# Kernel tuning notes

Measured on AMD Instinct MI355X. Metric: run time of the kernel, lower is better.

## Reference

```python
import jax, jax.numpy as jnp
import numpy as np

B, T, TR, DIM, H = 1, 4096, 1024, 1536, 12
DH = DIM // H          # 128
EPS = 1e-6             # RMSNorm eps
REF_SCALE = 1.0


def setup_inputs() -> dict:
    key = jax.random.key(0)
    ks = jax.random.split(key, 20)
    s = 0.02
    w = lambda k: jax.random.normal(k, (DIM, DIM), jnp.float32) * s
    b = lambda k: jax.random.normal(k, (DIM,), jnp.float32) * 0.01
    theta = jax.random.uniform(ks[2], (T, DH // 2), jnp.float32) * (2.0 * np.pi)
    return {
        "hidden_states": jax.random.normal(ks[0], (B, T, DIM), jnp.float32),
        "ref_hidden_states": jax.random.normal(ks[1], (B, TR, DIM), jnp.float32),
        "rot_cos": jnp.cos(theta),
        "rot_sin": jnp.sin(theta),
        "Wq": w(ks[3]), "bq": b(ks[4]),
        "Wk": w(ks[5]), "bk": b(ks[6]),
        "Wv": w(ks[7]), "bv": b(ks[8]),
        "Wkr": w(ks[9]), "bkr": b(ks[10]),
        "Wvr": w(ks[11]), "bvr": b(ks[12]),
        "Wo": w(ks[13]), "bo": b(ks[14]),
        "gq": jnp.ones((DIM,), jnp.float32),
        "gk": jnp.ones((DIM,), jnp.float32),
    }


def _rmsnorm(x, g):
    return x * jax.lax.rsqrt(jnp.mean(x * x, axis=-1, keepdims=True) + EPS) * g


def _heads(x):  # [B, T, DIM] -> [B, H, T, DH]
    return x.reshape(B, -1, H, DH).transpose(0, 2, 1, 3)


def _merge(x):  # [B, H, T, DH] -> [B, T, DIM]
    return x.transpose(0, 2, 1, 3).reshape(B, -1, DIM)


def _rope(x, c, s):
    # consecutive pairs along DH form complex numbers (view_as_complex semantics)
    xe, xo = x[..., 0::2], x[..., 1::2]
    c = c[None, None]  # [1,1,T,DH/2]
    s = s[None, None]
    re = xe * c - xo * s
    im = xe * s + xo * c
    return jnp.stack([re, im], axis=-1).reshape(x.shape)


def _attn(q, k, v):
    scale = 1.0 / jnp.sqrt(jnp.asarray(DH, q.dtype))
    p = jax.nn.softmax(jnp.einsum("bhqd,bhkd->bhqk", q, k) * scale, axis=-1)
    return jnp.einsum("bhqk,bhkd->bhqd", p, v)


def reference(hidden_states, ref_hidden_states, rot_cos, rot_sin,
              Wq, bq, Wk, bk, Wv, bv, Wkr, bkr, Wvr, bvr, Wo, bo, gq, gk):
    # QKV projections (self-attention: encoder_hidden_states = hidden_states)
    q_lin = hidden_states @ Wq + bq
    k_lin = hidden_states @ Wk + bk
    v_lin = hidden_states @ Wv + bv

    # ---- reference-attention branch (uses pre-RoPE query) ----
    ref_q = _heads(_rmsnorm(q_lin, gq))
    ref_k = _heads(_rmsnorm(ref_hidden_states @ Wkr + bkr, gk))
    ref_v = _heads(ref_hidden_states @ Wvr + bvr)
    ref_out = _merge(_attn(ref_q, ref_k, ref_v))  # [B, T, DIM]

    # ---- main attention with QK-norm + RoPE ----
    q = _rope(_heads(_rmsnorm(q_lin, gq)), rot_cos, rot_sin)
    k = _rope(_heads(_rmsnorm(k_lin, gk)), rot_cos, rot_sin)
    v = _heads(v_lin)
    main_out = _merge(_attn(q, k, v))  # [B, T, DIM]

    # scaled residual combine + output projection (dropout = identity)
    out = main_out + REF_SCALE * ref_out
    return out @ Wo + bo
```

## Files before the change

kernel.cpp:

```cpp
#include <hip/hip_runtime.h>

typedef unsigned short u16;
typedef unsigned int u32;
typedef __attribute__((ext_vector_type(8))) short short8;
typedef __attribute__((ext_vector_type(4))) float f32x4;

__device__ inline u16 f2b(float f) {
  u32 u = __builtin_bit_cast(u32, f);
  u += 0x7fff + ((u >> 16) & 1);
  return (u16)(u >> 16);
}
__device__ inline float b2f(u16 u) {
  return __builtin_bit_cast(float, (u32)u << 16);
}
__device__ inline u32 pack_bf16_rn(float a, float b) {
  const u32 ua = __builtin_bit_cast(u32, a) + 0x8000u;
  const u32 ub = __builtin_bit_cast(u32, b) + 0x8000u;
  return (ua >> 16) | (ub & 0xffff0000u);
}
__device__ inline void c_store(float* p, float v) { *p = v; }
__device__ inline void c_store(u16* p, float v) { *p = f2b(v); }

__device__ inline float fexp2(float x) {
#if __has_builtin(__builtin_amdgcn_exp2f)
  return __builtin_amdgcn_exp2f(x);
#else
  return exp2f(x);
#endif
}

typedef const __attribute__((address_space(1))) u32 gu32;
typedef __attribute__((address_space(3))) u32 lu32;
__device__ inline void async16(const u16* g, u16* l) {
  __builtin_amdgcn_global_load_lds((gu32*)g, (lu32*)l, 16, 0, 0);
}

#define QS (0.08838834764831843f * 1.4426950408889634f)

template <int MI, typename TC>
__global__ __launch_bounds__(256) void gemm128_kernel(
    const u16* __restrict__ A, long lda,
    const u16* __restrict__ Bt, long ldb,
    TC* __restrict__ C0, TC* __restrict__ C1, TC* __restrict__ C2, long ldc,
    const float* b0, const float* b1, const float* b2,
    int K) {
  __shared__ u16 As[32 * MI * 32];
  __shared__ u16 Bs[128 * 32];

  const int tid = threadIdx.x;
  const int lane = tid & 63;
  const int w = tid >> 6;
  const int r = lane & 15;
  const int quad = lane >> 4;
  const int m0 = blockIdx.y * (32 * MI);
  const int nb = blockIdx.x * 128;
  const int seg = nb / 1536;
  const int nc = nb - seg * 1536;
  TC* C = seg == 0 ? C0 : (seg == 1 ? C1 : C2);
  const float* bias = seg == 0 ? b0 : (seg == 1 ? b1 : b2);

  const int srow = lane >> 2;
  const int sx = ((lane & 3) ^ (srow & 3)) * 8;
  const u16* Ag = A + (size_t)(m0 + w * 8 * MI + srow) * lda + sx;
  const u16* Bg = Bt + (size_t)(nb + w * 32 + srow) * ldb + sx;
  u16* Al[MI / 2];
#pragma unroll
  for (int j = 0; j < MI / 2; ++j) Al[j] = &As[(w * 8 * MI + 16 * j) * 32];
  u16* const Bl0 = &Bs[(w * 32) * 32];
  u16* const Bl1 = &Bs[(w * 32 + 16) * 32];

  const int wm = (w >> 1) * (16 * MI);
  const int wn = (w & 1) * 64;

  f32x4 acc[MI][4];
#pragma unroll
  for (int i = 0; i < MI; ++i)
#pragma unroll
    for (int j = 0; j < 4; ++j) acc[i][j] = (f32x4){0.f, 0.f, 0.f, 0.f};

  const int fco = (quad ^ (r & 3)) * 8;

  for (int kk = 0; kk < K; kk += 32) {
    __syncthreads();
#pragma unroll
    for (int j = 0; j < MI / 2; ++j) async16(Ag + kk + (size_t)(16 * j) * lda, Al[j]);
    async16(Bg + kk, Bl0);
    async16(Bg + kk + 16 * ldb, Bl1);
    __syncthreads();

    short8 af[MI], bf[4];
#pragma unroll
    for (int mi = 0; mi < MI; ++mi)
      af[mi] = *reinterpret_cast<const short8*>(&As[(wm + 16 * mi + r) * 32 + fco]);
#pragma unroll
    for (int ni = 0; ni < 4; ++ni)
      bf[ni] = *reinterpret_cast<const short8*>(&Bs[(wn + 16 * ni + r) * 32 + fco]);
#pragma unroll
    for (int mi = 0; mi < MI; ++mi)
#pragma unroll
      for (int ni = 0; ni < 4; ++ni)
        acc[mi][ni] = __builtin_amdgcn_mfma_f32_16x16x32_bf16(af[mi], bf[ni], acc[mi][ni], 0, 0, 0);
  }

#pragma unroll
  for (int mi = 0; mi < MI; ++mi)
#pragma unroll
    for (int ni = 0; ni < 4; ++ni)
#pragma unroll
      for (int rr = 0; rr < 4; ++rr) {
        const int row = m0 + wm + 16 * mi + 4 * quad + rr;
        const int col = nc + wn + 16 * ni + r;
        c_store(&C[(size_t)row * ldc + col], acc[mi][ni][rr] + bias[col]);
      }
}

__global__ __launch_bounds__(256) void conv2_kernel(
    const float* __restrict__ xa, u16* __restrict__ ya, int n8a,
    const float* __restrict__ xb, u16* __restrict__ yb, int n8b) {
  int i = blockIdx.x * 256 + threadIdx.x;
  const float* x;
  u16* y;
  if (i < n8a) {
    x = xa; y = ya;
  } else {
    i -= n8a;
    if (i >= n8b) return;
    x = xb; y = yb;
  }
  const float4 v0 = reinterpret_cast<const float4*>(x)[2 * i];
  const float4 v1 = reinterpret_cast<const float4*>(x)[2 * i + 1];
  uint4 rv;
  rv.x = (u32)f2b(v0.x) | ((u32)f2b(v0.y) << 16);
  rv.y = (u32)f2b(v0.z) | ((u32)f2b(v0.w) << 16);
  rv.z = (u32)f2b(v1.x) | ((u32)f2b(v1.y) << 16);
  rv.w = (u32)f2b(v1.z) | ((u32)f2b(v1.w) << 16);
  reinterpret_cast<uint4*>(y)[i] = rv;
}

__device__ inline void transconv_body(const float* __restrict__ W, u16* __restrict__ Wt) {
  __shared__ u16 Ls[64 * 72];
  const int tid = threadIdx.x;
  const int k0 = blockIdx.y * 64;
  const int n0 = blockIdx.x * 64;
#pragma unroll
  for (int i = 0; i < 4; ++i) {
    const int c = tid + 256 * i;
    const int row = c >> 4;
    const int c4 = (c & 15) * 4;
    const float4 v = *reinterpret_cast<const float4*>(&W[(size_t)(k0 + row) * 1536 + n0 + c4]);
    Ls[(c4 + 0) * 72 + row] = f2b(v.x);
    Ls[(c4 + 1) * 72 + row] = f2b(v.y);
    Ls[(c4 + 2) * 72 + row] = f2b(v.z);
    Ls[(c4 + 3) * 72 + row] = f2b(v.w);
  }
  __syncthreads();
#pragma unroll
  for (int i = 0; i < 2; ++i) {
    const int c = tid + 256 * i;
    const int n = c >> 3;
    const int kc = (c & 7) * 8;
    u16 tmp[8];
#pragma unroll
    for (int j = 0; j < 8; ++j) tmp[j] = Ls[n * 72 + kc + j];
    *reinterpret_cast<uint4*>(&Wt[(size_t)(n0 + n) * 1536 + k0 + kc]) =
        *reinterpret_cast<const uint4*>(tmp);
  }
}

__global__ __launch_bounds__(256) void transconv6_kernel(
    const float* W0, const float* W1, const float* W2,
    const float* W3, const float* W4, const float* W5,
    u16* T0, u16* T1, u16* T2, u16* T3, u16* T4, u16* T5) {
  const int z = blockIdx.z;
  const float* W = z == 0 ? W0 : z == 1 ? W1 : z == 2 ? W2 : z == 3 ? W3 : z == 4 ? W4 : W5;
  u16* Wt = z == 0 ? T0 : z == 1 ? T1 : z == 2 ? T2 : z == 3 ? T3 : z == 4 ? T4 : T5;
  transconv_body(W, Wt);
}

__global__ __launch_bounds__(256) void rmsnorm3_kernel(
    const u16* xq, const u16* xk, const u16* xkr,
    const float* gq, const float* gk,
    const float* rc, const float* rs,
    u16* oq_plain, u16* oq_rope, u16* ok_rope, u16* okr_plain) {
  __shared__ float red[4];
  const int z = blockIdx.y;
  const int row = blockIdx.x;
  if (z == 2 && row >= 1024) return;
  const u16* x; const float* g; u16* po; u16* pr; float sc;
  if (z == 0)      { x = xq;  g = gq; po = oq_plain; pr = oq_rope; sc = QS;  }
  else if (z == 1) { x = xk;  g = gk; po = nullptr;  pr = ok_rope; sc = 1.f; }
  else             { x = xkr; g = gk; po = okr_plain; pr = nullptr; sc = 1.f; }

  const int tid = threadIdx.x;
  const u32* xr = reinterpret_cast<const u32*>(x + (size_t)row * 1536);
  float xe[3], xo[3];
  float ss = 0.f;
#pragma unroll
  for (int j = 0; j < 3; ++j) {
    const u32 u = xr[tid + 256 * j];
    const float e = b2f((u16)(u & 0xffff));
    const float o = b2f((u16)(u >> 16));
    xe[j] = e; xo[j] = o;
    ss += e * e + o * o;
  }
#pragma unroll
  for (int off = 32; off; off >>= 1) ss += __shfl_xor(ss, off, 64);
  if ((tid & 63) == 0) red[tid >> 6] = ss;
  __syncthreads();
  const float total = red[0] + red[1] + red[2] + red[3];
  const float rinv = rsqrtf(total * (1.0f / 1536.0f) + 1e-6f) * sc;
  u32* po32 = po ? reinterpret_cast<u32*>(po + (size_t)row * 1536) : nullptr;
  u32* pr32 = pr ? reinterpret_cast<u32*>(pr + (size_t)row * 1536) : nullptr;
#pragma unroll
  for (int j = 0; j < 3; ++j) {
    const int p = tid + 256 * j;
    const float2 gg = reinterpret_cast<const float2*>(g)[p];
    const float e = xe[j] * rinv * gg.x;
    const float o = xo[j] * rinv * gg.y;
    if (po32) po32[p] = (u32)f2b(e) | ((u32)f2b(o) << 16);
    if (pr32) {
      const int i = p & 63;
      const float c = rc[row * 64 + i];
      const float s = rs[row * 64 + i];
      const float re = e * c - o * s;
      const float im = e * s + o * c;
      pr32[p] = (u32)f2b(re) | ((u32)f2b(im) << 16);
    }
  }
}

__global__ __launch_bounds__(256) void vtrans2_kernel(
    const u16* __restrict__ V0, u16* __restrict__ Vt0,
    const u16* __restrict__ V1, u16* __restrict__ Vt1) {
  __shared__ u16 Ls[64 * 136];
  const int z = blockIdx.z;
  const int kvLen = z == 0 ? 4096 : 1024;
  const int kv0 = blockIdx.x * 64;
  if (kv0 >= kvLen) return;
  const u16* V = z == 0 ? V0 : V1;
  u16* Vt = z == 0 ? Vt0 : Vt1;
  const int tid = threadIdx.x;
  const int h = blockIdx.y;
#pragma unroll
  for (int i = 0; i < 4; ++i) {
    const int c = tid + 256 * i;
    const int row = c >> 4, c8 = c & 15;
    *reinterpret_cast<uint4*>(&Ls[row * 136 + 8 * c8]) =
        *reinterpret_cast<const uint4*>(V + (size_t)(kv0 + row) * 1536 + h * 128 + 8 * c8);
  }
  __syncthreads();
#pragma unroll
  for (int i = 0; i < 4; ++i) {
    const int c = tid + 256 * i;
    const int d = c >> 3, kc = c & 7;
    u16 tmp[8];
#pragma unroll
    for (int j = 0; j < 8; ++j) tmp[j] = Ls[(8 * kc + j) * 136 + d];
    *reinterpret_cast<uint4*>(Vt + ((size_t)h * 128 + d) * kvLen + kv0 + 8 * kc) =
        *reinterpret_cast<const uint4*>(tmp);
  }
}

__global__ __launch_bounds__(256) void flash2_kernel(
    const u16* __restrict__ Qc, const u16* __restrict__ Kc, const u16* __restrict__ Vtc,
    const u16* __restrict__ Qm, const u16* __restrict__ Km, const u16* __restrict__ Vtm,
    u16* __restrict__ Ob) {
  __shared__ u16 Ks[64 * 128];
  __shared__ u16 Vs[128 * 64];
  __shared__ u16 Pb[4][16 * 72];
  __shared__ float ab[4][16];

  const int tid = threadIdx.x;
  const int lane = tid & 63;
  const int w = tid >> 6;
  const int r = lane & 15;
  const int quad = lane >> 4;
  const int h = blockIdx.y;
  const int q0 = blockIdx.x * 64;
  const int qrow = q0 + 16 * w + r;
  const int sw = r & 7;

  f32x4 Ox[8];
#pragma unroll
  for (int dt = 0; dt < 8; ++dt) Ox[dt] = (f32x4){0.f, 0.f, 0.f, 0.f};

  for (int ph = 0; ph < 2; ++ph) {
    const u16* Q  = ph ? Qm : Qc;
    const u16* K  = ph ? Km : Kc;
    const u16* Vt = ph ? Vtm : Vtc;
    const int kvLen = ph ? 4096 : 1024;
    const int nt = kvLen >> 6;

    short8 qf[4];
    {
      const u16* qbase = Q + (size_t)qrow * 1536 + h * 128 + 8 * quad;
#pragma unroll
      for (int ks = 0; ks < 4; ++ks)
        qf[ks] = *reinterpret_cast<const short8*>(qbase + 32 * ks);
    }

    const u16* Vth = Vt + (size_t)h * 128 * kvLen;
    const u16* kg[4]; const u16* vg[4];
    u16* kl[4]; u16* vl[4];
    {
      const int p16 = lane & 15, rin = lane >> 4;
      const int p8 = lane & 7, din = lane >> 3;
#pragma unroll
      for (int j = 0; j < 4; ++j) {
        const int row = 16 * w + 4 * j + rin;
        kg[j] = K + (size_t)row * 1536 + h * 128 + 8 * (p16 ^ (row & 15));
        kl[j] = &Ks[(16 * w + 4 * j) * 128];
        const int d = 32 * w + 8 * j + din;
        vg[j] = Vth + (size_t)d * kvLen + 8 * (p8 ^ (d & 7));
        vl[j] = &Vs[(32 * w + 8 * j) * 64];
      }
    }

    f32x4 Oc[8];
#pragma unroll
    for (int dt = 0; dt < 8; ++dt) Oc[dt] = (f32x4){0.f, 0.f, 0.f, 0.f};
    float m_i = -1e30f, l_i = 0.f;

    for (int t = 0; t < nt; ++t) {
      __syncthreads();
      {
        const size_t ko = (size_t)t * 64 * 1536;
        const int vo = t * 64;
#pragma unroll
        for (int j = 0; j < 4; ++j) async16(kg[j] + ko, kl[j]);
#pragma unroll
        for (int j = 0; j < 4; ++j) async16(vg[j] + vo, vl[j]);
      }
      __syncthreads();

      f32x4 St[4];
#pragma unroll
      for (int mt = 0; mt < 4; ++mt) St[mt] = (f32x4){0.f, 0.f, 0.f, 0.f};
#pragma unroll
      for (int mt = 0; mt < 4; ++mt) {
        const u16* kp = &Ks[(16 * mt + r) * 128];
#pragma unroll
        for (int ks = 0; ks < 4; ++ks) {
          const short8 af = *reinterpret_cast<const short8*>(kp + 8 * ((quad + 4 * ks) ^ r));
          St[mt] = __builtin_amdgcn_mfma_f32_16x16x32_bf16(af, qf[ks], St[mt], 0, 0, 0);
        }
      }

      float mloc = -1e30f;
#pragma unroll
      for (int mt = 0; mt < 4; ++mt)
#pragma unroll
        for (int rr = 0; rr < 4; ++rr) mloc = fmaxf(mloc, St[mt][rr]);
      mloc = fmaxf(mloc, __shfl_xor(mloc, 16, 64));
      mloc = fmaxf(mloc, __shfl_xor(mloc, 32, 64));
      const float mn = fmaxf(m_i, mloc);

      float alpha = 1.0f;
      if (__any(mloc > m_i)) {
        alpha = fexp2(m_i - mn);
        if (quad == 0) ab[w][r] = alpha;
        const float4 a4 = *reinterpret_cast<const float4*>(&ab[w][4 * quad]);
#pragma unroll
        for (int dt = 0; dt < 8; ++dt) {
          Oc[dt][0] *= a4.x; Oc[dt][1] *= a4.y; Oc[dt][2] *= a4.z; Oc[dt][3] *= a4.w;
        }
      }

      float psum = 0.f;
      uint2 pk[4];
#pragma unroll
      for (int mt = 0; mt < 4; ++mt) {
        const float p0 = fexp2(St[mt][0] - mn);
        const float p1 = fexp2(St[mt][1] - mn);
        const float p2 = fexp2(St[mt][2] - mn);
        const float p3 = fexp2(St[mt][3] - mn);
        psum += (p0 + p1) + (p2 + p3);
        pk[mt].x = pack_bf16_rn(p0, p1);
        pk[mt].y = pack_bf16_rn(p2, p3);
      }
      psum += __shfl_xor(psum, 16, 64);
      psum += __shfl_xor(psum, 32, 64);
      l_i = l_i * alpha + psum;
      m_i = mn;

#pragma unroll
      for (int mt = 0; mt < 4; ++mt)
        *reinterpret_cast<uint2*>(&Pb[w][r * 72 + 16 * mt + 4 * quad]) = pk[mt];

      const short8 pa0 = *reinterpret_cast<const short8*>(&Pb[w][r * 72 + 8 * quad]);
      const short8 pa1 = *reinterpret_cast<const short8*>(&Pb[w][r * 72 + 32 + 8 * quad]);

#pragma unroll
      for (int dt = 0; dt < 8; ++dt) {
        const int d = 16 * dt + r;
        const short8 b0 = *reinterpret_cast<const short8*>(&Vs[d * 64 + 8 * (quad ^ sw)]);
        const short8 b1 = *reinterpret_cast<const short8*>(&Vs[d * 64 + 8 * ((4 + quad) ^ sw)]);
        Oc[dt] = __builtin_amdgcn_mfma_f32_16x16x32_bf16(pa0, b0, Oc[dt], 0, 0, 0);
        Oc[dt] = __builtin_amdgcn_mfma_f32_16x16x32_bf16(pa1, b1, Oc[dt], 0, 0, 0);
      }
    }

    if (quad == 0) ab[w][r] = 1.0f / l_i;
    const float4 li4 = *reinterpret_cast<const float4*>(&ab[w][4 * quad]);
    const float lv[4] = {li4.x, li4.y, li4.z, li4.w};
    if (ph == 0) {
#pragma unroll
      for (int dt = 0; dt < 8; ++dt)
#pragma unroll
        for (int rr = 0; rr < 4; ++rr) Ox[dt][rr] = Oc[dt][rr] * lv[rr];
    } else {
      u16* obb = Ob + (size_t)(q0 + 16 * w) * 1536 + h * 128;
#pragma unroll
      for (int rr = 0; rr < 4; ++rr) {
        u16* brow = obb + (size_t)(4 * quad + rr) * 1536 + r;
#pragma unroll
        for (int dt = 0; dt < 8; ++dt)
          brow[16 * dt] = f2b(Oc[dt][rr] * lv[rr] + Ox[dt][rr]);
      }
    }
  }
}

extern "C" void kernel_launch(void* const* d_in, const int* in_sizes, int n_in,
                              void* d_out, int out_size, void* d_ws, size_t ws_size,
                              hipStream_t stream) {
  (void)in_sizes; (void)n_in; (void)out_size; (void)ws_size;
  constexpr int T = 4096, TR = 1024, DIM = 1536, NH = 12;

  const float* hs  = (const float*)d_in[0];
  const float* rhs = (const float*)d_in[1];
  const float* rc  = (const float*)d_in[2];
  const float* rs  = (const float*)d_in[3];
  const float* Wq  = (const float*)d_in[4];
  const float* bq  = (const float*)d_in[5];
  const float* Wk  = (const float*)d_in[6];
  const float* bk  = (const float*)d_in[7];
  const float* Wv  = (const float*)d_in[8];
  const float* bv  = (const float*)d_in[9];
  const float* Wkr = (const float*)d_in[10];
  const float* bkr = (const float*)d_in[11];
  const float* Wvr = (const float*)d_in[12];
  const float* bvr = (const float*)d_in[13];
  const float* Wo  = (const float*)d_in[14];
  const float* bo  = (const float*)d_in[15];
  const float* gq  = (const float*)d_in[16];
  const float* gk  = (const float*)d_in[17];
  float* out = (float*)d_out;

  char* ws = (char*)d_ws;
  size_t off = 0;
  auto alloc = [&](size_t bytes) -> void* {
    void* p = ws + off;
    off += (bytes + 255) & ~(size_t)255;
    return p;
  };
  u16* bQ    = (u16*)alloc((size_t)T * DIM * 2);
  u16* bQr   = (u16*)alloc((size_t)T * DIM * 2);
  u16* bK    = (u16*)alloc((size_t)T * DIM * 2);
  u16* bV    = (u16*)alloc((size_t)T * DIM * 2);
  u16* bKr   = (u16*)alloc((size_t)TR * DIM * 2);
  u16* bVr   = (u16*)alloc((size_t)TR * DIM * 2);
  u16* bHs   = (u16*)alloc((size_t)T * DIM * 2);
  u16* bRhs  = (u16*)alloc((size_t)TR * DIM * 2);
  u16* bWqkv = (u16*)alloc((size_t)3 * DIM * DIM * 2);
  u16* bWr   = (u16*)alloc((size_t)2 * DIM * DIM * 2);
  u16* bWoT  = (u16*)alloc((size_t)DIM * DIM * 2);
  u16* VtG = bHs;
  u16* VtR = bRhs;
  u16* bOb = bWqkv;

  const dim3 blk(256);

  conv2_kernel<<<dim3((T * DIM / 8 + TR * DIM / 8 + 255) / 256), blk, 0, stream>>>(
      hs, bHs, T * DIM / 8, rhs, bRhs, TR * DIM / 8);

  transconv6_kernel<<<dim3(24, 24, 6), blk, 0, stream>>>(
      Wq, Wk, Wv, Wkr, Wvr, Wo,
      bWqkv + 0 * (size_t)DIM * DIM, bWqkv + 1 * (size_t)DIM * DIM,
      bWqkv + 2 * (size_t)DIM * DIM, bWr + 0 * (size_t)DIM * DIM,
      bWr + 1 * (size_t)DIM * DIM, bWoT);

  gemm128_kernel<4, u16><<<dim3(36, 32), blk, 0, stream>>>(
      bHs, DIM, bWqkv, DIM, bQ, bK, bV, DIM, bq, bk, bv, DIM);
  gemm128_kernel<2, u16><<<dim3(24, 16), blk, 0, stream>>>(
      bRhs, DIM, bWr, DIM, bKr, bVr, (u16*)nullptr, DIM, bkr, bvr, nullptr, DIM);

  rmsnorm3_kernel<<<dim3(T, 3), blk, 0, stream>>>(
      bQ, bK, bKr, gq, gk, rc, rs, bQ, bQr, bK, bKr);

  vtrans2_kernel<<<dim3(T / 64, NH, 2), blk, 0, stream>>>(bV, VtG, bVr, VtR);

  flash2_kernel<<<dim3(T / 64, NH), blk, 0, stream>>>(
      bQ, bKr, VtR, bQr, bK, VtG, bOb);

  gemm128_kernel<2, float><<<dim3(12, 64), blk, 0, stream>>>(
      bOb, DIM, bWoT, DIM, out, (float*)nullptr, (float*)nullptr, DIM, bo, nullptr, nullptr, DIM);
}
```

Baseline: 604.5 us.

## Split fused two-phase flash kernel into two launches with higher occupancy

Replaces the single flash kernel that ran both the reference and main attention phases (keeping an extra 8-register accumulator live across phases) with one kernel launched twice. The first launch writes the reference result to an fp32 workspace and the second adds it before the bf16 store. It also adds launch_bounds(256,4), halves the P staging buffer by processing it in two halves, and uses 32-bit offsets instead of pointer arrays, all aimed at lowering register and LDS pressure for more waves per CU. The cost is an extra launch plus a write and read of a 24MB fp32 intermediate.

```diff
diff --git a/kernel.cpp b/kernel.cpp
--- a/kernel.cpp
+++ b/kernel.cpp
@@ -261,13 +261,13 @@
   }
 }
 
-__global__ __launch_bounds__(256) void flash2_kernel(
-    const u16* __restrict__ Qc, const u16* __restrict__ Kc, const u16* __restrict__ Vtc,
-    const u16* __restrict__ Qm, const u16* __restrict__ Km, const u16* __restrict__ Vtm,
-    u16* __restrict__ Ob) {
+__global__ __launch_bounds__(256, 4) void flash_kernel(
+    const u16* __restrict__ Q, const u16* __restrict__ K,
+    const u16* __restrict__ Vt, float* __restrict__ O,
+    u16* __restrict__ Ob, int kvLen, int addO) {
   __shared__ u16 Ks[64 * 128];
   __shared__ u16 Vs[128 * 64];
-  __shared__ u16 Pb[4][16 * 72];
+  __shared__ u16 Pb[4][16 * 40];
   __shared__ float ab[4][16];
 
   const int tid = threadIdx.x;
@@ -280,142 +280,143 @@
   const int qrow = q0 + 16 * w + r;
   const int sw = r & 7;
 
-  f32x4 Ox[8];
-#pragma unroll
-  for (int dt = 0; dt < 8; ++dt) Ox[dt] = (f32x4){0.f, 0.f, 0.f, 0.f};
-
-  for (int ph = 0; ph < 2; ++ph) {
-    const u16* Q  = ph ? Qm : Qc;
-    const u16* K  = ph ? Km : Kc;
-    const u16* Vt = ph ? Vtm : Vtc;
-    const int kvLen = ph ? 4096 : 1024;
-    const int nt = kvLen >> 6;
-
-    short8 qf[4];
+  short8 qf[4];
+  {
+    const u16* qbase = Q + (size_t)qrow * 1536 + h * 128 + 8 * quad;
+#pragma unroll
+    for (int ks = 0; ks < 4; ++ks)
+      qf[ks] = *reinterpret_cast<const short8*>(qbase + 32 * ks);
+  }
+
+  const u16* Kb = K + h * 128;
+  const u16* Vb = Vt + (size_t)h * 128 * kvLen;
+  u32 koff[4], voff[4];
+  int klo[4], vlo[4];
+  {
+    const int p16 = lane & 15, rin = lane >> 4;
+    const int p8 = lane & 7, din = lane >> 3;
+#pragma unroll
+    for (int j = 0; j < 4; ++j) {
+      const int row = 16 * w + 4 * j + rin;
+      koff[j] = (u32)row * 1536u + 8u * (u32)(p16 ^ (row & 15));
+      klo[j] = (16 * w + 4 * j) * 128;
+      const int d = 32 * w + 8 * j + din;
+      voff[j] = (u32)d * (u32)kvLen + 8u * (u32)(p8 ^ (d & 7));
+      vlo[j] = (32 * w + 8 * j) * 64;
+    }
+  }
+
+  f32x4 Oc[8];
+#pragma unroll
+  for (int dt = 0; dt < 8; ++dt) Oc[dt] = (f32x4){0.f, 0.f, 0.f, 0.f};
+  float m_i = -1e30f, l_i = 0.f;
+
+  const int nt = kvLen >> 6;
+  for (int t = 0; t < nt; ++t) {
+    __syncthreads();
     {
-      const u16* qbase = Q + (size_t)qrow * 1536 + h * 128 + 8 * quad;
-#pragma unroll
-      for (int ks = 0; ks < 4; ++ks)
-        qf[ks] = *reinterpret_cast<const short8*>(qbase + 32 * ks);
-    }
-
-    const u16* Vth = Vt + (size_t)h * 128 * kvLen;
-    const u16* kg[4]; const u16* vg[4];
-    u16* kl[4]; u16* vl[4];
+      const size_t ko = (size_t)t * (64 * 1536);
+      const size_t vo = (size_t)t * 64;
+#pragma unroll
+      for (int j = 0; j < 4; ++j) async16(Kb + ko + koff[j], &Ks[klo[j]]);
+#pragma unroll
+      for (int j = 0; j < 4; ++j) async16(Vb + vo + voff[j], &Vs[vlo[j]]);
+    }
+    __syncthreads();
+
+    f32x4 St[4];
+#pragma unroll
+    for (int mt = 0; mt < 4; ++mt) St[mt] = (f32x4){0.f, 0.f, 0.f, 0.f};
+#pragma unroll
+    for (int mt = 0; mt < 4; ++mt) {
+      const u16* kp = &Ks[(16 * mt + r) * 128];
+#pragma unroll
+      for (int ks = 0; ks < 4; ++ks) {
+        const short8 af = *reinterpret_cast<const short8*>(kp + 8 * ((quad + 4 * ks) ^ r));
+        St[mt] = __builtin_amdgcn_mfma_f32_16x16x32_bf16(af, qf[ks], St[mt], 0, 0, 0);
+      }
+    }
+
+    float mloc = -1e30f;
+#pragma unroll
+    for (int mt = 0; mt < 4; ++mt)
+#pragma unroll
+      for (int rr = 0; rr < 4; ++rr) mloc = fmaxf(mloc, St[mt][rr]);
+    mloc = fmaxf(mloc, __shfl_xor(mloc, 16, 64));
+    mloc = fmaxf(mloc, __shfl_xor(mloc, 32, 64));
+    const float mn = fmaxf(m_i, mloc);
+
+    float alpha = 1.0f;
+    if (__any(mloc > m_i)) {
+      alpha = fexp2(m_i - mn);
+      if (quad == 0) ab[w][r] = alpha;
+      const float4 a4 = *reinterpret_cast<const float4*>(&ab[w][4 * quad]);
+#pragma unroll
+      for (int dt = 0; dt < 8; ++dt) {
+        Oc[dt][0] *= a4.x; Oc[dt][1] *= a4.y; Oc[dt][2] *= a4.z; Oc[dt][3] *= a4.w;
+      }
+    }
+
+    float psum = 0.f;
+    uint2 pk[4];
+#pragma unroll
+    for (int mt = 0; mt < 4; ++mt) {
+      const float p0 = fexp2(St[mt][0] - mn);
+      const float p1 = fexp2(St[mt][1] - mn);
+      const float p2 = fexp2(St[mt][2] - mn);
+      const float p3 = fexp2(St[mt][3] - mn);
+      psum += (p0 + p1) + (p2 + p3);
+      pk[mt].x = pack_bf16_rn(p0, p1);
+      pk[mt].y = pack_bf16_rn(p2, p3);
+    }
+    psum += __shfl_xor(psum, 16, 64);
+    psum += __shfl_xor(psum, 32, 64);
+    l_i = l_i * alpha + psum;
+    m_i = mn;
+
+#pragma unroll
+    for (int mt = 0; mt < 2; ++mt)
+      *reinterpret_cast<uint2*>(&Pb[w][r * 40 + 16 * mt + 4 * quad]) = pk[mt];
     {
-      const int p16 = lane & 15, rin = lane >> 4;
-      const int p8 = lane & 7, din = lane >> 3;
-#pragma unroll
-      for (int j = 0; j < 4; ++j) {
-        const int row = 16 * w + 4 * j + rin;
-        kg[j] = K + (size_t)row * 1536 + h * 128 + 8 * (p16 ^ (row & 15));
-        kl[j] = &Ks[(16 * w + 4 * j) * 128];
-        const int d = 32 * w + 8 * j + din;
-        vg[j] = Vth + (size_t)d * kvLen + 8 * (p8 ^ (d & 7));
-        vl[j] = &Vs[(32 * w + 8 * j) * 64];
-      }
-    }
-
-    f32x4 Oc[8];
-#pragma unroll
-    for (int dt = 0; dt < 8; ++dt) Oc[dt] = (f32x4){0.f, 0.f, 0.f, 0.f};
-    float m_i = -1e30f, l_i = 0.f;
-
-    for (int t = 0; t < nt; ++t) {
-      __syncthreads();
-      {
-        const size_t ko = (size_t)t * 64 * 1536;
-        const int vo = t * 64;
-#pragma unroll
-        for (int j = 0; j < 4; ++j) async16(kg[j] + ko, kl[j]);
-#pragma unroll
-        for (int j = 0; j < 4; ++j) async16(vg[j] + vo, vl[j]);
-      }
-      __syncthreads();
-
-      f32x4 St[4];
-#pragma unroll
-      for (int mt = 0; mt < 4; ++mt) St[mt] = (f32x4){0.f, 0.f, 0.f, 0.f};
-#pragma unroll
-      for (int mt = 0; mt < 4; ++mt) {
-        const u16* kp = &Ks[(16 * mt + r) * 128];
-#pragma unroll
-        for (int ks = 0; ks < 4; ++ks) {
-          const short8 af = *reinterpret_cast<const short8*>(kp + 8 * ((quad + 4 * ks) ^ r));
-          St[mt] = __builtin_amdgcn_mfma_f32_16x16x32_bf16(af, qf[ks], St[mt], 0, 0, 0);
-        }
-      }
-
-      float mloc = -1e30f;
-#pragma unroll
-      for (int mt = 0; mt < 4; ++mt)
-#pragma unroll
-        for (int rr = 0; rr < 4; ++rr) mloc = fmaxf(mloc, St[mt][rr]);
-      mloc = fmaxf(mloc, __shfl_xor(mloc, 16, 64));
-      mloc = fmaxf(mloc, __shfl_xor(mloc, 32, 64));
-      const float mn = fmaxf(m_i, mloc);
-
-      float alpha = 1.0f;
-      if (__any(mloc > m_i)) {
-        alpha = fexp2(m_i - mn);
-        if (quad == 0) ab[w][r] = alpha;
-        const float4 a4 = *reinterpret_cast<const float4*>(&ab[w][4 * quad]);
-#pragma unroll
-        for (int dt = 0; dt < 8; ++dt) {
-          Oc[dt][0] *= a4.x; Oc[dt][1] *= a4.y; Oc[dt][2] *= a4.z; Oc[dt][3] *= a4.w;
-        }
-      }
-
-      float psum = 0.f;
-      uint2 pk[4];
-#pragma unroll
-      for (int mt = 0; mt < 4; ++mt) {
-        const float p0 = fexp2(St[mt][0] - mn);
-        const float p1 = fexp2(St[mt][1] - mn);
-        const float p2 = fexp2(St[mt][2] - mn);
-        const float p3 = fexp2(St[mt][3] - mn);
-        psum += (p0 + p1) + (p2 + p3);
-        pk[mt].x = pack_bf16_rn(p0, p1);
-        pk[mt].y = pack_bf16_rn(p2, p3);
-      }
-      psum += __shfl_xor(psum, 16, 64);
-      psum += __shfl_xor(psum, 32, 64);
-      l_i = l_i * alpha + psum;
-      m_i = mn;
-
-#pragma unroll
-      for (int mt = 0; mt < 4; ++mt)
-        *reinterpret_cast<uint2*>(&Pb[w][r * 72 + 16 * mt + 4 * quad]) = pk[mt];
-
-      const short8 pa0 = *reinterpret_cast<const short8*>(&Pb[w][r * 72 + 8 * quad]);
-      const short8 pa1 = *reinterpret_cast<const short8*>(&Pb[w][r * 72 + 32 + 8 * quad]);
-
+      const short8 pa0 = *reinterpret_cast<const short8*>(&Pb[w][r * 40 + 8 * quad]);
 #pragma unroll
       for (int dt = 0; dt < 8; ++dt) {
         const int d = 16 * dt + r;
         const short8 b0 = *reinterpret_cast<const short8*>(&Vs[d * 64 + 8 * (quad ^ sw)]);
+        Oc[dt] = __builtin_amdgcn_mfma_f32_16x16x32_bf16(pa0, b0, Oc[dt], 0, 0, 0);
+      }
+    }
+#pragma unroll
+    for (int mt = 2; mt < 4; ++mt)
+      *reinterpret_cast<uint2*>(&Pb[w][r * 40 + 16 * (mt - 2) + 4 * quad]) = pk[mt];
+    {
+      const short8 pa1 = *reinterpret_cast<const short8*>(&Pb[w][r * 40 + 8 * quad]);
+#pragma unroll
+      for (int dt = 0; dt < 8; ++dt) {
+        const int d = 16 * dt + r;
         const short8 b1 = *reinterpret_cast<const short8*>(&Vs[d * 64 + 8 * ((4 + quad) ^ sw)]);
-        Oc[dt] = __builtin_amdgcn_mfma_f32_16x16x32_bf16(pa0, b0, Oc[dt], 0, 0, 0);
         Oc[dt] = __builtin_amdgcn_mfma_f32_16x16x32_bf16(pa1, b1, Oc[dt], 0, 0, 0);
       }
     }
-
-    if (quad == 0) ab[w][r] = 1.0f / l_i;
-    const float4 li4 = *reinterpret_cast<const float4*>(&ab[w][4 * quad]);
-    const float lv[4] = {li4.x, li4.y, li4.z, li4.w};
-    if (ph == 0) {
-#pragma unroll
-      for (int dt = 0; dt < 8; ++dt)
-#pragma unroll
-        for (int rr = 0; rr < 4; ++rr) Ox[dt][rr] = Oc[dt][rr] * lv[rr];
-    } else {
-      u16* obb = Ob + (size_t)(q0 + 16 * w) * 1536 + h * 128;
-#pragma unroll
-      for (int rr = 0; rr < 4; ++rr) {
-        u16* brow = obb + (size_t)(4 * quad + rr) * 1536 + r;
-#pragma unroll
-        for (int dt = 0; dt < 8; ++dt)
-          brow[16 * dt] = f2b(Oc[dt][rr] * lv[rr] + Ox[dt][rr]);
+  }
+
+  if (quad == 0) ab[w][r] = 1.0f / l_i;
+  const float4 li4 = *reinterpret_cast<const float4*>(&ab[w][4 * quad]);
+  const float lv[4] = {li4.x, li4.y, li4.z, li4.w};
+  float* obf = O + (size_t)(q0 + 16 * w) * 1536 + h * 128;
+  u16* obb = Ob + (size_t)(q0 + 16 * w) * 1536 + h * 128;
+#pragma unroll
+  for (int rr = 0; rr < 4; ++rr) {
+    float* orow = obf + (size_t)(4 * quad + rr) * 1536 + r;
+    u16* brow = obb + (size_t)(4 * quad + rr) * 1536 + r;
+#pragma unroll
+    for (int dt = 0; dt < 8; ++dt) {
+      float v = Oc[dt][rr] * lv[rr];
+      if (addO) {
+        v += orow[16 * dt];
+        brow[16 * dt] = f2b(v);
+      } else {
+        orow[16 * dt] = v;
       }
     }
   }
@@ -460,6 +461,7 @@
   u16* bV    = (u16*)alloc((size_t)T * DIM * 2);
   u16* bKr   = (u16*)alloc((size_t)TR * DIM * 2);
   u16* bVr   = (u16*)alloc((size_t)TR * DIM * 2);
+  float* bO  = (float*)alloc((size_t)T * DIM * 4);
   u16* bHs   = (u16*)alloc((size_t)T * DIM * 2);
   u16* bRhs  = (u16*)alloc((size_t)TR * DIM * 2);
   u16* bWqkv = (u16*)alloc((size_t)3 * DIM * DIM * 2);
@@ -490,8 +492,8 @@
 
   vtrans2_kernel<<<dim3(T / 64, NH, 2), blk, 0, stream>>>(bV, VtG, bVr, VtR);
 
-  flash2_kernel<<<dim3(T / 64, NH), blk, 0, stream>>>(
-      bQ, bKr, VtR, bQr, bK, VtG, bOb);
+  flash_kernel<<<dim3(T / 64, NH), blk, 0, stream>>>(bQ, bKr, VtR, bO, bOb, TR, 0);
+  flash_kernel<<<dim3(T / 64, NH), blk, 0, stream>>>(bQr, bK, VtG, bO, bOb, T, 1);
 
   gemm128_kernel<2, float><<<dim3(12, 64), blk, 0, stream>>>(
       bOb, DIM, bWoT, DIM, out, (float*)nullptr, (float*)nullptr, DIM, bo, nullptr, nullptr, DIM);
```

Result: faster. 546.7 us (-9.6%).
